# Performance work log

Hardware: AMD Instinct MI355X
Metric: run time of the kernel (lower is better)

The kernel has to match this reference:

```python
import jax, jax.numpy as jnp
import numpy as np

NUM_EMBEDS = 8192
EMBED_DIM = 256
BETA = 0.25


def setup_inputs() -> dict:
    key = jax.random.key(0)
    k1, k2 = jax.random.split(key)
    x_latent = jax.random.normal(k1, (16, EMBED_DIM, 32, 32), dtype=jnp.float32)
    # torch init: uniform(-1/num_embeds, 1/num_embeds)
    codebook = jax.random.uniform(
        k2, (NUM_EMBEDS, EMBED_DIM), dtype=jnp.float32,
        minval=-1.0 / NUM_EMBEDS, maxval=1.0 / NUM_EMBEDS)
    return {"x_latent": x_latent, "codebook": codebook}


def reference(x_latent, codebook):
    B, C, H, W = x_latent.shape  # C == EMBED_DIM
    # b c h w -> b (h w) c
    xf = x_latent.reshape(B, C, H * W).transpose(0, 2, 1)  # [B, N, D]
    x2 = jnp.sum(xf * xf, axis=-1, keepdims=True)            # [B, N, 1]
    e2 = jnp.sum(codebook * codebook, axis=-1)               # [E]
    xe = jnp.einsum('bnd,ed->bne', xf, codebook)             # [B, N, E]
    dist = x2 + e2[None, None, :] - 2.0 * xe
    encoding_inds = jnp.argmin(dist, axis=-1)                # [B, N] int
    quantized = jnp.take(codebook, encoding_inds, axis=0)    # [B, N, D]
    # b (h w) d -> b d h w
    quantized = quantized.transpose(0, 2, 1).reshape(B, C, H, W)
    commitment_loss = jnp.mean((jax.lax.stop_gradient(quantized) - x_latent) ** 2)
    embedding_loss = jnp.mean((quantized - jax.lax.stop_gradient(x_latent)) ** 2)
    vq_loss = commitment_loss * BETA + embedding_loss
    # straight-through estimator
    quantized_st = x_latent + jax.lax.stop_gradient(quantized - x_latent)
    return (quantized_st, vq_loss)
```

## Files before the change

### kernel.cpp

```cpp
#include <hip/hip_runtime.h>
#include <hip/hip_bf16.h>

typedef int   i4v  __attribute__((ext_vector_type(4)));
typedef int   i8v  __attribute__((ext_vector_type(8)));
typedef float f16v __attribute__((ext_vector_type(16)));

#define NUM_EMBEDS 8192
#define EMBED_DIM  256
#define BATCH      16
#define HW         1024
#define NVEC       (BATCH * HW)
#define OUT0_ELEMS (BATCH * EMBED_DIM * HW)
#define NSPLIT     8
#define COLS_PER_S 1024
#define NTILES     32

#define BUFB  8192
#define E2L   24576
#define SMEM3 28672

#define SCORE_BIAS 2097152.0f
#define SCALE_ONE 0x7F7F7F7F

#define WS_XQ   0
#define WS_EQ   4194304
#define WS_E2   6291456
#define WS_AMIN 6324224
#define WS_LOSS 6455296

static __device__ __forceinline__ void gload_lds16(const void* g, void* l) {
    __builtin_amdgcn_global_load_lds(
        (const __attribute__((address_space(1))) unsigned int*)g,
        (__attribute__((address_space(3))) unsigned int*)l, 16, 0, 0);
}

static __device__ __forceinline__ unsigned pk_fp8x4(float a, float b, float c, float d) {
    int w = __builtin_amdgcn_cvt_pk_fp8_f32(a, b, 0, false);
    w = __builtin_amdgcn_cvt_pk_fp8_f32(c, d, w, true);
    return (unsigned)w;
}

__global__ void k_prep(const float* __restrict__ x, const float* __restrict__ cb,
                       unsigned char* __restrict__ xq, unsigned char* __restrict__ eq,
                       float* __restrict__ e2, unsigned long long* __restrict__ amin,
                       float* __restrict__ loss) {
    const int tx = threadIdx.x;
    const int ty = threadIdx.y;
    const int tid = ty * 32 + tx;

    if (blockIdx.z == 16) {
        const int bid = blockIdx.y * 32 + blockIdx.x;
        const int row = bid * 32 + (tid >> 3);
        const int sub = tid & 7;
        const float4* src = reinterpret_cast<const float4*>(cb + (size_t)row * 256 + sub * 32);
        float s = 0.f;
        unsigned ou[8];
        #pragma unroll
        for (int i = 0; i < 4; ++i) {
            const float4 a = src[2 * i], b = src[2 * i + 1];
            s = fmaf(a.x, a.x, s); s = fmaf(a.y, a.y, s);
            s = fmaf(a.z, a.z, s); s = fmaf(a.w, a.w, s);
            s = fmaf(b.x, b.x, s); s = fmaf(b.y, b.y, s);
            s = fmaf(b.z, b.z, s); s = fmaf(b.w, b.w, s);
            ou[2 * i]     = pk_fp8x4(a.x * 8192.f, a.y * 8192.f, a.z * 8192.f, a.w * 8192.f);
            ou[2 * i + 1] = pk_fp8x4(b.x * 8192.f, b.y * 8192.f, b.z * 8192.f, b.w * 8192.f);
        }
        uint4* dst = reinterpret_cast<uint4*>(eq + (size_t)row * 256 + sub * 32);
        dst[0] = make_uint4(ou[0], ou[1], ou[2], ou[3]);
        dst[1] = make_uint4(ou[4], ou[5], ou[6], ou[7]);
        s += __shfl_xor(s, 1, 64);
        s += __shfl_xor(s, 2, 64);
        s += __shfl_xor(s, 4, 64);
        if (sub == 0) e2[row] = fmaf(s, 67108864.0f, SCORE_BIAS);
        return;
    }

    __shared__ float t[32][33];
    const int hw0 = blockIdx.x * 32;
    const int c0  = blockIdx.y * 32;
    const int b   = blockIdx.z;
    if (blockIdx.z == 0 && blockIdx.y < 2) {
        const int i = (blockIdx.y * 32 + blockIdx.x) * 256 + tid;
        amin[i] = ~0ULL;
        if (i == 0) *loss = 0.0f;
    }
    #pragma unroll
    for (int i = 0; i < 4; ++i) {
        const int c = c0 + ty + i * 8;
        t[ty + i * 8][tx] = x[((b * EMBED_DIM + c) << 10) + hw0 + tx];
    }
    __syncthreads();
    {
        const unsigned w = pk_fp8x4(t[ty * 4 + 0][tx], t[ty * 4 + 1][tx],
                                    t[ty * 4 + 2][tx], t[ty * 4 + 3][tx]);
        const int n = (b << 10) + hw0 + tx;
        *reinterpret_cast<unsigned*>(xq + (size_t)n * 256 + c0 + ty * 4) = w;
    }
}

__global__ void __launch_bounds__(256, 2)
k_argmin(const unsigned char* __restrict__ xq, const unsigned char* __restrict__ eq,
         const float* __restrict__ e2, unsigned long long* __restrict__ amin) {
    extern __shared__ char smem[];
    const int tid  = threadIdx.x;
    const int lane = tid & 63;
    const int w    = tid >> 6;
    const int l31  = lane & 31;
    const int hi   = lane >> 5;
    const int s    = blockIdx.x & 7;
    const int rb   = blockIdx.x >> 3;
    const int row0 = rb * 256;
    const int cb0  = s * COLS_PER_S;

    const char* xqB = (const char*)xq;
    const char* eqB = (const char*)eq;
    const char* e2B = (const char*)e2;

    i8v afr[2][4];
    #pragma unroll
    for (int mr = 0; mr < 2; ++mr) {
        const int arow = row0 + w * 64 + mr * 32 + l31;
        const char* ap = xqB + ((size_t)arow << 8) + hi * 32;
        #pragma unroll
        for (int ks = 0; ks < 4; ++ks) {
            const i4v lo  = *reinterpret_cast<const i4v*>(ap + ks * 64);
            const i4v hi4 = *reinterpret_cast<const i4v*>(ap + ks * 64 + 16);
            afr[mr][ks] = (i8v){lo.x, lo.y, lo.z, lo.w, hi4.x, hi4.y, hi4.z, hi4.w};
        }
    }

    gload_lds16(e2B + ((size_t)cb0 << 2) + w * 1024 + lane * 16,
                smem + E2L + w * 1024);

    auto STAGE = [&](int tci, int lds_off) {
        #pragma unroll
        for (int j = 0; j < 2; ++j) {
            const int p = w * 2 + j;
            const int r = 4 * p + (lane >> 4);
            const int c = (lane & 15) ^ (r & 7);
            gload_lds16(eqB + ((size_t)(cb0 + tci * 32 + r) << 8) + (c << 4),
                        smem + lds_off + p * 1024);
        }
    };
    STAGE(0, 0);
    STAGE(1, BUFB);

    #pragma unroll
    for (int mr = 0; mr < 2; ++mr)
        #pragma unroll
        for (int ks = 0; ks < 4; ++ks)
            asm volatile("" : "+v"(afr[mr][ks]));

    unsigned mu0[16], mu1[16];
    #pragma unroll
    for (int r = 0; r < 16; ++r) { mu0[r] = 0xFFFFFFFFu; mu1[r] = 0xFFFFFFFFu; }

    const int sx = l31 & 7;

    auto PHASE = [&](int t, f16v& c0v, f16v& c1v, float& evS, unsigned& orvS) {
        if (t < NTILES - 1) {
            asm volatile("s_waitcnt vmcnt(2)" ::: "memory");
        } else {
            asm volatile("s_waitcnt vmcnt(0)" ::: "memory");
        }
        __builtin_amdgcn_s_barrier();
        if (t + 2 < NTILES) STAGE(t + 2, ((t + 2) % 3) * BUFB);

        evS  = *reinterpret_cast<const float*>(smem + E2L + t * 128 + l31 * 4);
        orvS = (unsigned)((t << 5) | l31);
        const char* bb = smem + (t % 3) * BUFB + l31 * 256;

        c0v = (f16v){}; c1v = (f16v){};
        __builtin_amdgcn_s_setprio(1);
        #pragma unroll
        for (int ks = 0; ks < 4; ++ks) {
            const int cc0 = (4 * ks + 2 * hi) ^ sx;
            const int cc1 = (4 * ks + 2 * hi + 1) ^ sx;
            const i4v lo  = *reinterpret_cast<const i4v*>(bb + (cc0 << 4));
            const i4v hi4 = *reinterpret_cast<const i4v*>(bb + (cc1 << 4));
            const i8v bf = (i8v){lo.x, lo.y, lo.z, lo.w, hi4.x, hi4.y, hi4.z, hi4.w};
            c0v = __builtin_amdgcn_mfma_scale_f32_32x32x64_f8f6f4(
                      afr[0][ks], bf, c0v, 0, 0, 0, SCALE_ONE, 0, SCALE_ONE);
            c1v = __builtin_amdgcn_mfma_scale_f32_32x32x64_f8f6f4(
                      afr[1][ks], bf, c1v, 0, 0, 0, SCALE_ONE, 0, SCALE_ONE);
        }
        __builtin_amdgcn_s_setprio(0);
    };

    auto EPI = [&](const f16v& c0v, const f16v& c1v, float evS, unsigned orvS) {
        #pragma unroll
        for (int r = 0; r < 16; ++r) {
            const float s0 = fmaf(-16384.0f, c0v[r], evS);
            mu0[r] = min(mu0[r], (__float_as_uint(s0) & 0xFFFFFC00u) | orvS);
            const float s1 = fmaf(-16384.0f, c1v[r], evS);
            mu1[r] = min(mu1[r], (__float_as_uint(s1) & 0xFFFFFC00u) | orvS);
        }
    };

    f16v aA0, aA1, aB0, aB1;
    float evA, evB; unsigned orvA, orvB;
    PHASE(0, aA0, aA1, evA, orvA);
    for (int t = 1; t < NTILES - 1; t += 2) {
        PHASE(t,     aB0, aB1, evB, orvB);  EPI(aA0, aA1, evA, orvA);
        PHASE(t + 1, aA0, aA1, evA, orvA);  EPI(aB0, aB1, evB, orvB);
    }
    PHASE(NTILES - 1, aB0, aB1, evB, orvB);
    EPI(aA0, aA1, evA, orvA);
    EPI(aB0, aB1, evB, orvB);

    #pragma unroll
    for (int mr = 0; mr < 2; ++mr)
        #pragma unroll
        for (int r = 0; r < 16; ++r) {
            unsigned u = mr ? mu1[r] : mu0[r];
            #pragma unroll
            for (int m = 1; m <= 16; m <<= 1)
                u = min(u, (unsigned)__shfl_xor((int)u, m, 64));
            if (l31 == 0) {
                const int row_g = row0 + w * 64 + mr * 32 + (r & 3) + 8 * (r >> 2) + 4 * hi;
                const int col = cb0 + (int)(u & 1023u);
                const unsigned long long key = ((unsigned long long)u << 32) | (unsigned)col;
                atomicMin(&amin[row_g], key);
            }
        }
}

__global__ void __launch_bounds__(256)
k_gather_loss(const float* __restrict__ x, const float* __restrict__ cb,
              const unsigned long long* __restrict__ amin, float* __restrict__ out,
              float* __restrict__ loss) {
    __shared__ float q[32][257];
    __shared__ int e_s[32];
    const int tid = threadIdx.x;
    const int hw0 = (blockIdx.x & 31) * 32;
    const int b   = blockIdx.x >> 5;
    const int n0  = (b << 10) + hw0;
    if (tid < 32) e_s[tid] = (int)(amin[n0 + tid] & 0xFFFFFFFFu);
    __syncthreads();
    #pragma unroll 8
    for (int r = 0; r < 32; ++r)
        q[r][tid] = cb[(size_t)e_s[r] * EMBED_DIM + tid];
    __syncthreads();
    const int tx = tid & 31;
    const int ty = tid >> 5;
    float sum = 0.f;
    #pragma unroll
    for (int i = 0; i < 32; ++i) {
        const int c = ty * 32 + i;
        const float qv = q[tx][c];
        const int o = ((b * EMBED_DIM + c) << 10) + hw0 + tx;
        const float xv = x[o];
        out[o] = qv;
        const float d = qv - xv;
        sum = fmaf(d, d, sum);
    }
    #pragma unroll
    for (int off = 32; off > 0; off >>= 1) sum += __shfl_down(sum, off, 64);
    __shared__ float ls[4];
    const int lane = tid & 63, wid = tid >> 6;
    if (lane == 0) ls[wid] = sum;
    __syncthreads();
    if (tid == 0) atomicAdd(loss, ls[0] + ls[1] + ls[2] + ls[3]);
}

__global__ void k_finalize(const float* __restrict__ loss, float* __restrict__ out) {
    out[OUT0_ELEMS] = loss[0] * (1.25f / (float)OUT0_ELEMS);
}

extern "C" void kernel_launch(void* const* d_in, const int* in_sizes, int n_in,
                              void* d_out, int out_size, void* d_ws, size_t ws_size,
                              hipStream_t stream) {
    const float* x  = (const float*)d_in[0];
    const float* cb = (const float*)d_in[1];
    float* out = (float*)d_out;

    char* ws = (char*)d_ws;
    unsigned char* xq = (unsigned char*)(ws + WS_XQ);
    unsigned char* eq = (unsigned char*)(ws + WS_EQ);
    float* e2 = (float*)(ws + WS_E2);
    unsigned long long* amin = (unsigned long long*)(ws + WS_AMIN);
    float* loss = (float*)(ws + WS_LOSS);

    k_prep<<<dim3(32, 8, 17), dim3(32, 8, 1), 0, stream>>>(x, cb, xq, eq, e2, amin, loss);
    k_argmin<<<dim3(64 * NSPLIT), dim3(256), SMEM3, stream>>>(xq, eq, e2, amin);
    k_gather_loss<<<dim3(512), dim3(256), 0, stream>>>(x, cb, amin, out, loss);
    k_finalize<<<dim3(1), dim3(1), 0, stream>>>(loss, out);
}
```

Baseline: 66.33 us.

## Stage two codebook tiles per barrier and fold loss finalize into gather kernel

The argmin kernel now loads 64 codebook rows per pipeline phase, triple-buffered in doubled LDS slots. That halves the number of barriers and waitcnt points, and the MFMA bursts for the two 32-column sub-tiles are interleaved with the epilogue of the previous sub-tile. The separate single-thread finalize kernel is removed: the last gather block, detected with an atomic counter, writes the scaled loss. The larger LDS footprint (about 52KB) may limit occupancy to two blocks per CU, and the counter adds a threadfence and atomic per block.

```diff
diff --git a/kernel.cpp b/kernel.cpp
--- a/kernel.cpp
+++ b/kernel.cpp
@@ -13,11 +13,11 @@
 #define OUT0_ELEMS (BATCH * EMBED_DIM * HW)
 #define NSPLIT     8
 #define COLS_PER_S 1024
-#define NTILES     32
-
-#define BUFB  8192
-#define E2L   24576
-#define SMEM3 28672
+#define NPHASE     16
+
+#define BUF2  16384
+#define E2L   49152
+#define SMEM3 53248
 
 #define SCORE_BIAS 2097152.0f
 #define SCALE_ONE 0x7F7F7F7F
@@ -27,6 +27,7 @@
 #define WS_E2   6291456
 #define WS_AMIN 6324224
 #define WS_LOSS 6455296
+#define WS_CNT  6455300
 
 static __device__ __forceinline__ void gload_lds16(const void* g, void* l) {
     __builtin_amdgcn_global_load_lds(
@@ -43,7 +44,7 @@
 __global__ void k_prep(const float* __restrict__ x, const float* __restrict__ cb,
                        unsigned char* __restrict__ xq, unsigned char* __restrict__ eq,
                        float* __restrict__ e2, unsigned long long* __restrict__ amin,
-                       float* __restrict__ loss) {
+                       float* __restrict__ loss, unsigned* __restrict__ cnt) {
     const int tx = threadIdx.x;
     const int ty = threadIdx.y;
     const int tid = ty * 32 + tx;
@@ -82,7 +83,7 @@
     if (blockIdx.z == 0 && blockIdx.y < 2) {
         const int i = (blockIdx.y * 32 + blockIdx.x) * 256 + tid;
         amin[i] = ~0ULL;
-        if (i == 0) *loss = 0.0f;
+        if (i == 0) { *loss = 0.0f; *cnt = 0u; }
     }
     #pragma unroll
     for (int i = 0; i < 4; ++i) {
@@ -132,18 +133,18 @@
     gload_lds16(e2B + ((size_t)cb0 << 2) + w * 1024 + lane * 16,
                 smem + E2L + w * 1024);
 
-    auto STAGE = [&](int tci, int lds_off) {
-        #pragma unroll
-        for (int j = 0; j < 2; ++j) {
-            const int p = w * 2 + j;
+    auto STAGE = [&](int ph, int lds_off) {
+        #pragma unroll
+        for (int j = 0; j < 4; ++j) {
+            const int p = w * 4 + j;
             const int r = 4 * p + (lane >> 4);
             const int c = (lane & 15) ^ (r & 7);
-            gload_lds16(eqB + ((size_t)(cb0 + tci * 32 + r) << 8) + (c << 4),
+            gload_lds16(eqB + ((size_t)(cb0 + ph * 64 + r) << 8) + (c << 4),
                         smem + lds_off + p * 1024);
         }
     };
     STAGE(0, 0);
-    STAGE(1, BUFB);
+    STAGE(1, BUF2);
 
     #pragma unroll
     for (int mr = 0; mr < 2; ++mr)
@@ -157,19 +158,18 @@
 
     const int sx = l31 & 7;
 
-    auto PHASE = [&](int t, f16v& c0v, f16v& c1v, float& evS, unsigned& orvS) {
-        if (t < NTILES - 1) {
-            asm volatile("s_waitcnt vmcnt(2)" ::: "memory");
+    auto SYNC = [&](int ph) {
+        if (ph < NPHASE - 1) {
+            asm volatile("s_waitcnt vmcnt(4)" ::: "memory");
         } else {
             asm volatile("s_waitcnt vmcnt(0)" ::: "memory");
         }
         __builtin_amdgcn_s_barrier();
-        if (t + 2 < NTILES) STAGE(t + 2, ((t + 2) % 3) * BUFB);
-
-        evS  = *reinterpret_cast<const float*>(smem + E2L + t * 128 + l31 * 4);
-        orvS = (unsigned)((t << 5) | l31);
-        const char* bb = smem + (t % 3) * BUFB + l31 * 256;
-
+        if (ph + 2 < NPHASE) STAGE(ph + 2, ((ph + 2) % 3) * BUF2);
+    };
+
+    auto BURST = [&](int ph, int h, f16v& c0v, f16v& c1v) {
+        const char* bb = smem + (ph % 3) * BUF2 + h * 8192 + l31 * 256;
         c0v = (f16v){}; c1v = (f16v){};
         __builtin_amdgcn_s_setprio(1);
         #pragma unroll
@@ -187,7 +187,9 @@
         __builtin_amdgcn_s_setprio(0);
     };
 
-    auto EPI = [&](const f16v& c0v, const f16v& c1v, float evS, unsigned orvS) {
+    auto EPI = [&](const f16v& c0v, const f16v& c1v, int st) {
+        const float evS = *reinterpret_cast<const float*>(smem + E2L + st * 128 + l31 * 4);
+        const unsigned orvS = (unsigned)((st << 5) | l31);
         #pragma unroll
         for (int r = 0; r < 16; ++r) {
             const float s0 = fmaf(-16384.0f, c0v[r], evS);
@@ -197,16 +199,19 @@
         }
     };
 
-    f16v aA0, aA1, aB0, aB1;
-    float evA, evB; unsigned orvA, orvB;
-    PHASE(0, aA0, aA1, evA, orvA);
-    for (int t = 1; t < NTILES - 1; t += 2) {
-        PHASE(t,     aB0, aB1, evB, orvB);  EPI(aA0, aA1, evA, orvA);
-        PHASE(t + 1, aA0, aA1, evA, orvA);  EPI(aB0, aB1, evB, orvB);
-    }
-    PHASE(NTILES - 1, aB0, aB1, evB, orvB);
-    EPI(aA0, aA1, evA, orvA);
-    EPI(aB0, aB1, evB, orvB);
+    f16v X0, X1, Y0, Y1;
+    SYNC(0);
+    BURST(0, 0, X0, X1);
+    BURST(0, 1, Y0, Y1);
+    EPI(X0, X1, 0);
+    for (int ph = 1; ph < NPHASE; ++ph) {
+        SYNC(ph);
+        BURST(ph, 0, X0, X1);
+        EPI(Y0, Y1, 2 * ph - 1);
+        BURST(ph, 1, Y0, Y1);
+        EPI(X0, X1, 2 * ph);
+    }
+    EPI(Y0, Y1, 2 * NPHASE - 1);
 
     #pragma unroll
     for (int mr = 0; mr < 2; ++mr)
@@ -228,7 +233,7 @@
 __global__ void __launch_bounds__(256)
 k_gather_loss(const float* __restrict__ x, const float* __restrict__ cb,
               const unsigned long long* __restrict__ amin, float* __restrict__ out,
-              float* __restrict__ loss) {
+              float* __restrict__ loss, unsigned* __restrict__ cnt) {
     __shared__ float q[32][257];
     __shared__ int e_s[32];
     const int tid = threadIdx.x;
@@ -260,11 +265,14 @@
     const int lane = tid & 63, wid = tid >> 6;
     if (lane == 0) ls[wid] = sum;
     __syncthreads();
-    if (tid == 0) atomicAdd(loss, ls[0] + ls[1] + ls[2] + ls[3]);
-}
-
-__global__ void k_finalize(const float* __restrict__ loss, float* __restrict__ out) {
-    out[OUT0_ELEMS] = loss[0] * (1.25f / (float)OUT0_ELEMS);
+    if (tid == 0) {
+        atomicAdd(loss, ls[0] + ls[1] + ls[2] + ls[3]);
+        __threadfence();
+        if (atomicAdd(cnt, 1u) == 511u) {
+            const float tot = atomicAdd(loss, 0.0f);
+            out[OUT0_ELEMS] = tot * (1.25f / (float)OUT0_ELEMS);
+        }
+    }
 }
 
 extern "C" void kernel_launch(void* const* d_in, const int* in_sizes, int n_in,
@@ -280,9 +288,9 @@
     float* e2 = (float*)(ws + WS_E2);
     unsigned long long* amin = (unsigned long long*)(ws + WS_AMIN);
     float* loss = (float*)(ws + WS_LOSS);
-
-    k_prep<<<dim3(32, 8, 17), dim3(32, 8, 1), 0, stream>>>(x, cb, xq, eq, e2, amin, loss);
+    unsigned* cnt = (unsigned*)(ws + WS_CNT);
+
+    k_prep<<<dim3(32, 8, 17), dim3(32, 8, 1), 0, stream>>>(x, cb, xq, eq, e2, amin, loss, cnt);
     k_argmin<<<dim3(64 * NSPLIT), dim3(256), SMEM3, stream>>>(xq, eq, e2, amin);
-    k_gather_loss<<<dim3(512), dim3(256), 0, stream>>>(x, cb, amin, out, loss);
-    k_finalize<<<dim3(1), dim3(1), 0, stream>>>(loss, out);
-}
+    k_gather_loss<<<dim3(512), dim3(256), 0, stream>>>(x, cb, amin, out, loss, cnt);
+}
```

New measurement: 85.01 us. 1.28x slower.
